# Kernel tuning notes

Measured on AMD Instinct MI355X. Metric: run time of the kernel, lower is better.

## Reference

```python
import jax, jax.numpy as jnp
import numpy as np

LN_EPS = 1e-5

def layer_norm(x, g, b):
    mu = jnp.mean(x, axis=-1, keepdims=True)
    var = jnp.var(x, axis=-1, keepdims=True)
    return (x - mu) * jax.lax.rsqrt(var + LN_EPS) * g + b

def setup_inputs() -> dict:
    key = jax.random.key(0)
    ks = jax.random.split(key, 4)
    d = 2048
    bs, win_len, obj_num = 8, 64, 36
    return {
        "visual_feats": jax.random.normal(ks[0], (bs, win_len, d), dtype=jnp.float32),
        "obj_feats": jax.random.normal(ks[1], (bs, win_len, obj_num, d), dtype=jnp.float32),
        "W_v": jax.random.normal(ks[2], (d, d), dtype=jnp.float32) * (1.0 / np.sqrt(d)),
        "b_v": jnp.zeros((d,), dtype=jnp.float32),
        "W_o": jax.random.normal(ks[3], (d, d), dtype=jnp.float32) * (1.0 / np.sqrt(d)),
        "b_o": jnp.zeros((d,), dtype=jnp.float32),
        "ln_v_g": jnp.ones((d,), dtype=jnp.float32),
        "ln_v_b": jnp.zeros((d,), dtype=jnp.float32),
        "ln_o_g": jnp.ones((d,), dtype=jnp.float32),
        "ln_o_b": jnp.zeros((d,), dtype=jnp.float32),
        "ln_ov_g": jnp.ones((d,), dtype=jnp.float32),
        "ln_ov_b": jnp.zeros((d,), dtype=jnp.float32),
    }

def reference(visual_feats, obj_feats, W_v, b_v, W_o, b_o,
              ln_v_g, ln_v_b, ln_o_g, ln_o_b, ln_ov_g, ln_ov_b):
    bs, win_len, obj_num, obj_size = obj_feats.shape
    # visual branch: linear -> tanh -> LN   [bs, F, d]
    ve = layer_norm(jnp.tanh(visual_feats @ W_v + b_v), ln_v_g, ln_v_b)
    # object branch: linear -> flatten frames*objects -> tanh -> LN  [bs, N, d]
    oe = (obj_feats @ W_o + b_o).reshape(bs, win_len * obj_num, obj_size)
    oe = layer_norm(jnp.tanh(oe), ln_o_g, ln_o_b)
    # adjacency: [bs, N, F], softmax over N (object axis, dim=1)
    adj = jnp.einsum('bnd,bfd->bnf', oe, ve) / jnp.sqrt(jnp.asarray(obj_size, dtype=oe.dtype))
    adj = jax.nn.softmax(adj, axis=1)
    # aggregate objects per frame: (oe^T @ adj)^T -> [bs, F, d]
    obj_agg = jnp.einsum('bnd,bnf->bfd', oe, adj)
    return layer_norm(jnp.tanh(obj_agg + ve), ln_ov_g, ln_ov_b)
```

## Files before the change

### kernel.cpp

```cpp
#include <hip/hip_runtime.h>
#include <cstdint>
#include <cstddef>


typedef __attribute__((ext_vector_type(4))) float f32x4;
typedef __attribute__((ext_vector_type(4))) unsigned int u32x4;
typedef __attribute__((ext_vector_type(8))) short bf16x8;

#define DD 2048
#define BS 8
#define FF 64
#define NOBJ 2304
#define MO 18432
#define MV 512

__device__ __forceinline__ unsigned short f2bf(float f) {
  unsigned int u = __float_as_uint(f);
  u += 0x7fffu + ((u >> 16) & 1u);
  return (unsigned short)(u >> 16);
}
__device__ __forceinline__ unsigned int pk2(float a, float b) {
  return (unsigned int)f2bf(a) | ((unsigned int)f2bf(b) << 16);
}

typedef __attribute__((address_space(1))) const unsigned int gas_u32;
typedef __attribute__((address_space(3))) unsigned int las_u32;
__device__ __forceinline__ void gl_lds16(const void* g, void* l) {
  __builtin_amdgcn_global_load_lds((gas_u32*)g, (las_u32*)l, 16, 0, 0);
}

__global__ __launch_bounds__(256) void k_cvt_bf16(const float* __restrict__ X,
                                                  unsigned short* __restrict__ O,
                                                  int n16) {
  int idx = blockIdx.x * 256 + threadIdx.x;
  const int stride = gridDim.x * 256;
  for (int i = idx; i < n16; i += stride) {
    const f32x4* src = (const f32x4*)(X + (size_t)i * 16);
    f32x4 a = src[0], b = src[1], c = src[2], d = src[3];
    u32x4 p = {pk2(a.x, a.y), pk2(a.z, a.w), pk2(b.x, b.y), pk2(b.z, b.w)};
    u32x4 q = {pk2(c.x, c.y), pk2(c.z, c.w), pk2(d.x, d.y), pk2(d.z, d.w)};
    u32x4* dst = (u32x4*)(O + (size_t)i * 16);
    dst[0] = p;
    dst[1] = q;
  }
}

__global__ __launch_bounds__(256) void k_wprep(const float* __restrict__ W,
                                               unsigned short* __restrict__ Wt) {
  __shared__ unsigned short sh[64][65];
  const int t = threadIdx.x;
  const int kb = blockIdx.x * 64, nb = blockIdx.y * 64;
  {
    const int rk = t >> 2, seg = t & 3;
    const float* src = W + (size_t)(kb + rk) * DD + nb + seg * 16;
#pragma unroll
    for (int q = 0; q < 4; ++q) {
      f32x4 x = *(const f32x4*)(src + q * 4);
      sh[rk][seg * 16 + q * 4 + 0] = f2bf(x.x);
      sh[rk][seg * 16 + q * 4 + 1] = f2bf(x.y);
      sh[rk][seg * 16 + q * 4 + 2] = f2bf(x.z);
      sh[rk][seg * 16 + q * 4 + 3] = f2bf(x.w);
    }
  }
  __syncthreads();
  {
    const int nn = t >> 2, ks = t & 3;
    unsigned int o[8];
#pragma unroll
    for (int j = 0; j < 8; ++j)
      o[j] = (unsigned int)sh[ks * 16 + 2 * j][nn] |
             ((unsigned int)sh[ks * 16 + 2 * j + 1][nn] << 16);
    u32x4 p0 = {o[0], o[1], o[2], o[3]};
    u32x4 p1 = {o[4], o[5], o[6], o[7]};
    unsigned short* dst = Wt + (size_t)(nb + nn) * DD + kb + ks * 16;
    ((u32x4*)dst)[0] = p0;
    ((u32x4*)dst)[1] = p1;
  }
}

__global__ __launch_bounds__(256) void k_gemm_bb(const unsigned short* __restrict__ A,
                                                 const unsigned short* __restrict__ Bt,
                                                 const float* __restrict__ bias,
                                                 float* __restrict__ Y) {
  __shared__ __align__(16) unsigned short As[128 * 32];
  __shared__ __align__(16) unsigned short Bs[128 * 32];
  const int t = threadIdx.x;
  const int lane = t & 63, wave = t >> 6;
  const int r = lane & 15, g = lane >> 4;
  const int wm = wave >> 1, wn = wave & 1;
  const int nwg = gridDim.x * gridDim.y;
  const int orig = blockIdx.y * gridDim.x + blockIdx.x;
  const int per = nwg >> 3;
  const int lin = (orig & 7) * per + (orig >> 3);
  const int bm = (lin >> 4) * 128;
  const int bn = (lin & 15) * 128;

  const int srow = t >> 2, scol = (t & 3) * 8;
  const unsigned short* agp = A + (size_t)(bm + srow) * DD + scol;
  const unsigned short* bgp = Bt + (size_t)(bn + srow) * DD + scol;
  unsigned short* alds0 = As + t * 8;
  unsigned short* alds1 = As + 2048 + t * 8;
  unsigned short* blds0 = Bs + t * 8;
  unsigned short* blds1 = Bs + 2048 + t * 8;

  f32x4 acc[4][4] = {};
  for (int kt = 0; kt < DD / 32; ++kt) {
    const int kb = kt * 32;
    gl_lds16(agp + kb, alds0);
    gl_lds16(agp + kb + (size_t)64 * DD, alds1);
    gl_lds16(bgp + kb, blds0);
    gl_lds16(bgp + kb + (size_t)64 * DD, blds1);
    __syncthreads();
    bf16x8 af[4], bfr[4];
#pragma unroll
    for (int m = 0; m < 4; ++m)
      af[m] = *(const bf16x8*)(As + (wm * 64 + m * 16 + r) * 32 + g * 8);
#pragma unroll
    for (int n = 0; n < 4; ++n)
      bfr[n] = *(const bf16x8*)(Bs + (wn * 64 + n * 16 + r) * 32 + g * 8);
#pragma unroll
    for (int m = 0; m < 4; ++m)
#pragma unroll
      for (int n = 0; n < 4; ++n)
        acc[m][n] = __builtin_amdgcn_mfma_f32_16x16x32_bf16(af[m], bfr[n], acc[m][n], 0, 0, 0);
    __syncthreads();
  }
#pragma unroll
  for (int m = 0; m < 4; ++m) {
    const int row0 = bm + wm * 64 + m * 16 + g * 4;
#pragma unroll
    for (int n = 0; n < 4; ++n) {
      const int col = bn + wn * 64 + n * 16 + r;
      const float bv = bias[col];
#pragma unroll
      for (int i = 0; i < 4; ++i)
        Y[(size_t)(row0 + i) * DD + col] = acc[m][n][i] + bv;
    }
  }
}

__global__ __launch_bounds__(256) void k_gemm_xw(const float* __restrict__ X,
                                                 const unsigned short* __restrict__ Wt,
                                                 const float* __restrict__ bias,
                                                 float* __restrict__ Y) {
  __shared__ __align__(16) unsigned short As[128 * 32];
  __shared__ __align__(16) unsigned short Bs[128 * 32];
  const int t = threadIdx.x;
  const int lane = t & 63, wave = t >> 6;
  const int r = lane & 15, g = lane >> 4;
  const int wm = wave >> 1, wn = wave & 1;
  const int bm = blockIdx.y * 128, bn = blockIdx.x * 128;
  const int arow = t >> 1, ah = t & 1;
  f32x4 acc[4][4] = {};
  const float* aptr = X + (size_t)(bm + arow) * DD + ah * 16;
  const unsigned short* bptr = Wt + (size_t)(bn + arow) * DD + ah * 16;
  for (int kt = 0; kt < DD / 32; ++kt) {
    const int kb = kt * 32;
    f32x4 a0 = *(const f32x4*)(aptr + kb);
    f32x4 a1 = *(const f32x4*)(aptr + kb + 4);
    f32x4 a2 = *(const f32x4*)(aptr + kb + 8);
    f32x4 a3 = *(const f32x4*)(aptr + kb + 12);
    u32x4 b0 = *(const u32x4*)(bptr + kb);
    u32x4 b1 = *(const u32x4*)(bptr + kb + 8);
    __syncthreads();
    u32x4 p0 = {pk2(a0.x, a0.y), pk2(a0.z, a0.w), pk2(a1.x, a1.y), pk2(a1.z, a1.w)};
    u32x4 p1 = {pk2(a2.x, a2.y), pk2(a2.z, a2.w), pk2(a3.x, a3.y), pk2(a3.z, a3.w)};
    ((u32x4*)As)[arow * 4 + ah * 2 + 0] = p0;
    ((u32x4*)As)[arow * 4 + ah * 2 + 1] = p1;
    ((u32x4*)Bs)[arow * 4 + ah * 2 + 0] = b0;
    ((u32x4*)Bs)[arow * 4 + ah * 2 + 1] = b1;
    __syncthreads();
    bf16x8 af[4], bfr[4];
#pragma unroll
    for (int m = 0; m < 4; ++m) af[m] = ((const bf16x8*)As)[(wm * 64 + m * 16 + r) * 4 + g];
#pragma unroll
    for (int n = 0; n < 4; ++n) bfr[n] = ((const bf16x8*)Bs)[(wn * 64 + n * 16 + r) * 4 + g];
#pragma unroll
    for (int m = 0; m < 4; ++m)
#pragma unroll
      for (int n = 0; n < 4; ++n)
        acc[m][n] = __builtin_amdgcn_mfma_f32_16x16x32_bf16(af[m], bfr[n], acc[m][n], 0, 0, 0);
  }
#pragma unroll
  for (int m = 0; m < 4; ++m) {
    const int row0 = bm + wm * 64 + m * 16 + g * 4;
#pragma unroll
    for (int n = 0; n < 4; ++n) {
      const int col = bn + wn * 64 + n * 16 + r;
      const float bv = bias[col];
#pragma unroll
      for (int i = 0; i < 4; ++i)
        Y[(size_t)(row0 + i) * DD + col] = acc[m][n][i] + bv;
    }
  }
}

__global__ __launch_bounds__(256) void k_ep_ln(const float* __restrict__ Y,
                                               const float* __restrict__ Y2,
                                               const float* __restrict__ gw,
                                               const float* __restrict__ bw,
                                               unsigned short* __restrict__ obf,
                                               float* __restrict__ of32) {
  const int row = blockIdx.x, t = threadIdx.x;
  const size_t base = (size_t)row * DD + t * 8;
  f32x4 v0 = ((const f32x4*)(Y + base))[0];
  f32x4 v1 = ((const f32x4*)(Y + base))[1];
  if (Y2 != nullptr) {
    v0 += ((const f32x4*)(Y2 + base))[0];
    v1 += ((const f32x4*)(Y2 + base))[1];
  }
  float tv[8];
#pragma unroll
  for (int j = 0; j < 4; ++j) {
    tv[j] = tanhf(v0[j]);
    tv[4 + j] = tanhf(v1[j]);
  }
  float s1 = 0.f, s2 = 0.f;
#pragma unroll
  for (int j = 0; j < 8; ++j) {
    s1 += tv[j];
    s2 += tv[j] * tv[j];
  }
#pragma unroll
  for (int m = 1; m < 64; m <<= 1) {
    s1 += __shfl_xor(s1, m, 64);
    s2 += __shfl_xor(s2, m, 64);
  }
  __shared__ float r1[4], r2[4];
  const int wave = t >> 6;
  if ((t & 63) == 0) {
    r1[wave] = s1;
    r2[wave] = s2;
  }
  __syncthreads();
  const float S1 = r1[0] + r1[1] + r1[2] + r1[3];
  const float S2 = r2[0] + r2[1] + r2[2] + r2[3];
  const float mean = S1 * (1.0f / DD);
  const float var = S2 * (1.0f / DD) - mean * mean;
  const float rstd = rsqrtf(var + 1e-5f);
  f32x4 g0 = ((const f32x4*)(gw + t * 8))[0], g1 = ((const f32x4*)(gw + t * 8))[1];
  f32x4 bb0 = ((const f32x4*)(bw + t * 8))[0], bb1 = ((const f32x4*)(bw + t * 8))[1];
  float o[8];
#pragma unroll
  for (int j = 0; j < 4; ++j) {
    o[j] = (tv[j] - mean) * rstd * g0[j] + bb0[j];
    o[4 + j] = (tv[4 + j] - mean) * rstd * g1[j] + bb1[j];
  }
  if (obf != nullptr) {
    u32x4 p = {pk2(o[0], o[1]), pk2(o[2], o[3]), pk2(o[4], o[5]), pk2(o[6], o[7])};
    *((u32x4*)(obf + base)) = p;
  }
  if (of32 != nullptr) {
    f32x4 w0 = {o[0], o[1], o[2], o[3]}, w1 = {o[4], o[5], o[6], o[7]};
    ((f32x4*)(of32 + base))[0] = w0;
    ((f32x4*)(of32 + base))[1] = w1;
  }
}

__global__ __launch_bounds__(256) void k_troe(const unsigned short* __restrict__ oe,
                                              unsigned short* __restrict__ oeT) {
  __shared__ unsigned short sh[64][65];
  const int t = threadIdx.x;
  const int b = blockIdx.z, nt = blockIdx.x, dt = blockIdx.y;
  {
    const int nn = t >> 2, seg = t & 3;
    const unsigned short* src = oe + ((size_t)b * NOBJ + nt * 64 + nn) * DD + dt * 64 + seg * 16;
    u32x4 x0 = ((const u32x4*)src)[0];
    u32x4 x1 = ((const u32x4*)src)[1];
    const unsigned short* px0 = (const unsigned short*)&x0;
    const unsigned short* px1 = (const unsigned short*)&x1;
#pragma unroll
    for (int j = 0; j < 8; ++j) {
      sh[nn][seg * 16 + j] = px0[j];
      sh[nn][seg * 16 + 8 + j] = px1[j];
    }
  }
  __syncthreads();
  {
    const int dd = t >> 2, ns = t & 3;
    unsigned int o[8];
#pragma unroll
    for (int j = 0; j < 8; ++j)
      o[j] = (unsigned int)sh[ns * 16 + 2 * j][dd] |
             ((unsigned int)sh[ns * 16 + 2 * j + 1][dd] << 16);
    u32x4 p0 = {o[0], o[1], o[2], o[3]};
    u32x4 p1 = {o[4], o[5], o[6], o[7]};
    unsigned short* dst = oeT + ((size_t)b * DD + dt * 64 + dd) * NOBJ + nt * 64 + ns * 16;
    ((u32x4*)dst)[0] = p0;
    ((u32x4*)dst)[1] = p1;
  }
}

__global__ __launch_bounds__(256) void k_gemm_adj(const unsigned short* __restrict__ oe,
                                                  const unsigned short* __restrict__ veb,
                                                  float* __restrict__ adjT) {
  __shared__ __align__(16) unsigned short As[128 * 32];
  __shared__ __align__(16) unsigned short Bs[64 * 32];
  const int t = threadIdx.x;
  const int lane = t & 63, wave = t >> 6;
  const int r = lane & 15, g = lane >> 4;
  const int wm = wave >> 1, wn = wave & 1;
  const int b = blockIdx.y, bm = blockIdx.x * 128;
  const int arow = t >> 1, ah = t & 1;
  const int br_ = t >> 2, bseg = t & 3;
  f32x4 acc[4][2] = {};
  const unsigned short* aptr = oe + ((size_t)b * NOBJ + bm + arow) * DD + ah * 16;
  const unsigned short* bptr = veb + ((size_t)b * FF + br_) * DD + bseg * 8;
  for (int kt = 0; kt < DD / 32; ++kt) {
    const int kb = kt * 32;
    u32x4 a0 = ((const u32x4*)(aptr + kb))[0];
    u32x4 a1 = ((const u32x4*)(aptr + kb))[1];
    u32x4 bv = *(const u32x4*)(bptr + kb);
    __syncthreads();
    ((u32x4*)As)[arow * 4 + ah * 2 + 0] = a0;
    ((u32x4*)As)[arow * 4 + ah * 2 + 1] = a1;
    ((u32x4*)Bs)[br_ * 4 + bseg] = bv;
    __syncthreads();
    bf16x8 af[4], bfr[2];
#pragma unroll
    for (int m = 0; m < 4; ++m) af[m] = ((const bf16x8*)As)[(wm * 64 + m * 16 + r) * 4 + g];
#pragma unroll
    for (int n = 0; n < 2; ++n) bfr[n] = ((const bf16x8*)Bs)[(wn * 32 + n * 16 + r) * 4 + g];
#pragma unroll
    for (int m = 0; m < 4; ++m)
#pragma unroll
      for (int n = 0; n < 2; ++n)
        acc[m][n] = __builtin_amdgcn_mfma_f32_16x16x32_bf16(af[m], bfr[n], acc[m][n], 0, 0, 0);
  }
  const float scale = 0.02209708691207961f;
#pragma unroll
  for (int m = 0; m < 4; ++m)
#pragma unroll
    for (int n = 0; n < 2; ++n) {
      const int f = wn * 32 + n * 16 + r;
      const int n0 = bm + wm * 64 + m * 16 + g * 4;
      f32x4 v = acc[m][n];
      v *= scale;
      *(f32x4*)(adjT + ((size_t)b * FF + f) * NOBJ + n0) = v;
    }
}

__global__ __launch_bounds__(256) void k_smax(const float* __restrict__ adjT,
                                              unsigned short* __restrict__ out) {
  const int t = threadIdx.x;
  const size_t base = (size_t)blockIdx.x * NOBJ;
  float v[9];
#pragma unroll
  for (int j = 0; j < 9; ++j) v[j] = adjT[base + t + j * 256];
  float m = v[0];
#pragma unroll
  for (int j = 1; j < 9; ++j) m = fmaxf(m, v[j]);
#pragma unroll
  for (int s = 1; s < 64; s <<= 1) m = fmaxf(m, __shfl_xor(m, s, 64));
  __shared__ float rm[4], rs[4];
  const int wave = t >> 6;
  if ((t & 63) == 0) rm[wave] = m;
  __syncthreads();
  m = fmaxf(fmaxf(rm[0], rm[1]), fmaxf(rm[2], rm[3]));
  float e[9];
  float s = 0.f;
#pragma unroll
  for (int j = 0; j < 9; ++j) {
    e[j] = __expf(v[j] - m);
    s += e[j];
  }
#pragma unroll
  for (int q = 1; q < 64; q <<= 1) s += __shfl_xor(s, q, 64);
  if ((t & 63) == 0) rs[wave] = s;
  __syncthreads();
  const float S = rs[0] + rs[1] + rs[2] + rs[3];
  const float inv = 1.0f / S;
#pragma unroll
  for (int j = 0; j < 9; ++j) out[base + t + j * 256] = f2bf(e[j] * inv);
}

__global__ __launch_bounds__(256) void k_gemm_agg(const unsigned short* __restrict__ adjsm,
                                                  const unsigned short* __restrict__ oeT,
                                                  float* __restrict__ agg) {
  __shared__ __align__(16) unsigned short As[64 * 32];
  __shared__ __align__(16) unsigned short Bs[128 * 32];
  const int t = threadIdx.x;
  const int lane = t & 63, wave = t >> 6;
  const int r = lane & 15, g = lane >> 4;
  const int wm = wave >> 1, wn = wave & 1;
  const int b = blockIdx.y, bn = blockIdx.x * 128;
  const int ar = t >> 2, aseg = t & 3;
  const int brow = t >> 1, bh = t & 1;
  f32x4 acc[2][4] = {};
  const unsigned short* aptr = adjsm + ((size_t)b * FF + ar) * NOBJ + aseg * 8;
  const unsigned short* bptr = oeT + ((size_t)b * DD + bn + brow) * NOBJ + bh * 16;
  for (int kt = 0; kt < NOBJ / 32; ++kt) {
    const int kb = kt * 32;
    u32x4 av = *(const u32x4*)(aptr + kb);
    u32x4 b0 = ((const u32x4*)(bptr + kb))[0];
    u32x4 b1 = ((const u32x4*)(bptr + kb))[1];
    __syncthreads();
    ((u32x4*)As)[ar * 4 + aseg] = av;
    ((u32x4*)Bs)[brow * 4 + bh * 2 + 0] = b0;
    ((u32x4*)Bs)[brow * 4 + bh * 2 + 1] = b1;
    __syncthreads();
    bf16x8 af[2], bfr[4];
#pragma unroll
    for (int m = 0; m < 2; ++m) af[m] = ((const bf16x8*)As)[(wm * 32 + m * 16 + r) * 4 + g];
#pragma unroll
    for (int n = 0; n < 4; ++n) bfr[n] = ((const bf16x8*)Bs)[(wn * 64 + n * 16 + r) * 4 + g];
#pragma unroll
    for (int m = 0; m < 2; ++m)
#pragma unroll
      for (int n = 0; n < 4; ++n)
        acc[m][n] = __builtin_amdgcn_mfma_f32_16x16x32_bf16(af[m], bfr[n], acc[m][n], 0, 0, 0);
  }
#pragma unroll
  for (int m = 0; m < 2; ++m)
#pragma unroll
    for (int n = 0; n < 4; ++n) {
      const int d = bn + wn * 64 + n * 16 + r;
#pragma unroll
      for (int i = 0; i < 4; ++i) {
        const int f = wm * 32 + m * 16 + g * 4 + i;
        agg[((size_t)b * FF + f) * DD + d] = acc[m][n][i];
      }
    }
}


extern "C" void kernel_launch(void* const* d_in, const int* in_sizes, int n_in,
                              void* d_out, int out_size, void* d_ws, size_t ws_size,
                              hipStream_t stream) {
  (void)in_sizes; (void)n_in; (void)out_size;
  const float* visual = (const float*)d_in[0];
  const float* obj    = (const float*)d_in[1];
  const float* W_v    = (const float*)d_in[2];
  const float* b_v    = (const float*)d_in[3];
  const float* W_o    = (const float*)d_in[4];
  const float* b_o    = (const float*)d_in[5];
  const float* ln_v_g = (const float*)d_in[6];
  const float* ln_v_b = (const float*)d_in[7];
  const float* ln_o_g = (const float*)d_in[8];
  const float* ln_o_b = (const float*)d_in[9];
  const float* ln_ov_g = (const float*)d_in[10];
  const float* ln_ov_b = (const float*)d_in[11];

  char* ws = (char*)d_ws;
  constexpr size_t OFF_WVT = 0;
  constexpr size_t OFF_WOT = 8ull << 20;
  constexpr size_t OFF_OBJB = 16ull << 20;
  constexpr size_t OFF_YO  = 88ull << 20;
  constexpr size_t OFF_YV  = 232ull << 20;
  constexpr size_t OFF_VEF = 236ull << 20;
  constexpr size_t OFF_VEB = 240ull << 20;
  constexpr size_t OFF_ADJ = 242ull << 20;
  constexpr size_t OFF_ADJS = OFF_ADJ + 4718592ull;
  constexpr size_t OFF_AGG = OFF_ADJS + 2359296ull;
  constexpr size_t WS_NEED = OFF_AGG + 4194304ull;
  if (ws_size < WS_NEED) return;

  unsigned short* WvT  = (unsigned short*)(ws + OFF_WVT);
  unsigned short* WoT  = (unsigned short*)(ws + OFF_WOT);
  unsigned short* objb = (unsigned short*)(ws + OFF_OBJB);
  unsigned short* oe_b = (unsigned short*)(ws + OFF_OBJB);
  float* Yo            = (float*)(ws + OFF_YO);
  unsigned short* oeT  = (unsigned short*)(ws + OFF_YO);
  float* Yv            = (float*)(ws + OFF_YV);
  float* ve_f          = (float*)(ws + OFF_VEF);
  unsigned short* ve_b = (unsigned short*)(ws + OFF_VEB);
  float* adjT          = (float*)(ws + OFF_ADJ);
  unsigned short* adjs = (unsigned short*)(ws + OFF_ADJS);
  float* agg           = (float*)(ws + OFF_AGG);

  dim3 b256(256);
  k_wprep<<<dim3(32, 32), b256, 0, stream>>>(W_v, WvT);
  k_wprep<<<dim3(32, 32), b256, 0, stream>>>(W_o, WoT);
  k_cvt_bf16<<<dim3(2048), b256, 0, stream>>>(obj, objb, MO * DD / 16);
  k_gemm_xw<<<dim3(16, MV / 128), b256, 0, stream>>>(visual, WvT, b_v, Yv);
  k_gemm_bb<<<dim3(16, MO / 128), b256, 0, stream>>>(objb, WoT, b_o, Yo);
  k_ep_ln<<<dim3(MV), b256, 0, stream>>>(Yv, nullptr, ln_v_g, ln_v_b, ve_b, ve_f);
  k_ep_ln<<<dim3(MO), b256, 0, stream>>>(Yo, nullptr, ln_o_g, ln_o_b, oe_b, nullptr);
  k_troe<<<dim3(36, 32, 8), b256, 0, stream>>>(oe_b, oeT);
  k_gemm_adj<<<dim3(NOBJ / 128, BS), b256, 0, stream>>>(oe_b, ve_b, adjT);
  k_smax<<<dim3(MV), b256, 0, stream>>>(adjT, adjs);
  k_gemm_agg<<<dim3(DD / 128, BS), b256, 0, stream>>>(adjs, oeT, agg);
  k_ep_ln<<<dim3(MV), b256, 0, stream>>>(agg, ve_f, ln_ov_g, ln_ov_b, nullptr, (float*)d_out);
}
```

Before: 461.6 us.

## Triple-buffer the object GEMM with swizzled LDS and larger 256x128 tiles

Rewrites the main bf16 object-projection GEMM to use 512-thread blocks over 256x128 output tiles with K-step 64. Global-to-LDS loads are triple-buffered and issued two stages ahead, with explicit vmcnt waits and a single barrier per iteration, so memory traffic overlaps the MFMA work. The LDS layout is XOR-swizzled to avoid bank conflicts, and wave priority is raised around the MFMA block. In exchange the kernel uses about 144KB of LDS, which limits it to one block per CU, and it depends on hand-tuned waitcnt counts being correct.

```diff
diff --git a/kernel.cpp b/kernel.cpp
--- a/kernel.cpp
+++ b/kernel.cpp
@@ -78,63 +78,103 @@
   }
 }
 
-__global__ __launch_bounds__(256) void k_gemm_bb(const unsigned short* __restrict__ A,
-                                                 const unsigned short* __restrict__ Bt,
-                                                 const float* __restrict__ bias,
-                                                 float* __restrict__ Y) {
-  __shared__ __align__(16) unsigned short As[128 * 32];
-  __shared__ __align__(16) unsigned short Bs[128 * 32];
-  const int t = threadIdx.x;
-  const int lane = t & 63, wave = t >> 6;
+__global__ __launch_bounds__(512, 1) void k_gemm_bb(const unsigned short* __restrict__ A,
+                                                    const unsigned short* __restrict__ Bt,
+                                                    const float* __restrict__ bias,
+                                                    float* __restrict__ Y) {
+  __shared__ __align__(16) unsigned short lds[3 * 24576];
+  const int tid = threadIdx.x;
+  const int lane = tid & 63, wave = tid >> 6;
   const int r = lane & 15, g = lane >> 4;
   const int wm = wave >> 1, wn = wave & 1;
+
   const int nwg = gridDim.x * gridDim.y;
   const int orig = blockIdx.y * gridDim.x + blockIdx.x;
   const int per = nwg >> 3;
   const int lin = (orig & 7) * per + (orig >> 3);
-  const int bm = (lin >> 4) * 128;
+  const int bm = (lin >> 4) * 256;
   const int bn = (lin & 15) * 128;
 
-  const int srow = t >> 2, scol = (t & 3) * 8;
-  const unsigned short* agp = A + (size_t)(bm + srow) * DD + scol;
-  const unsigned short* bgp = Bt + (size_t)(bn + srow) * DD + scol;
-  unsigned short* alds0 = As + t * 8;
-  unsigned short* alds1 = As + 2048 + t * 8;
-  unsigned short* blds0 = Bs + t * 8;
-  unsigned short* blds1 = Bs + 2048 + t * 8;
+  const int srow = tid >> 3;
+  const int k16s = (tid & 7) ^ (srow & 7);
+  const unsigned short* aSrc[4];
+#pragma unroll
+  for (int q = 0; q < 4; ++q)
+    aSrc[q] = A + (size_t)(bm + q * 64 + srow) * DD + k16s * 8;
+  const unsigned short* bSrc[2];
+#pragma unroll
+  for (int q = 0; q < 2; ++q)
+    bSrc[q] = Bt + (size_t)(bn + q * 64 + srow) * DD + k16s * 8;
+
+  const int rs = r & 7;
+  const int sa0 = ((0 + g) ^ rs) * 8;
+  const int sa1 = ((4 + g) ^ rs) * 8;
+  const int arow0 = wm * 64 + r;
+  const int brow0 = wn * 64 + r;
+
+  auto stage = [&](int buf, int kt) {
+    unsigned short* ab = lds + buf * 24576;
+    unsigned short* bb = ab + 16384;
+    const size_t ko = (size_t)kt * 64;
+#pragma unroll
+    for (int q = 0; q < 4; ++q)
+      gl_lds16(aSrc[q] + ko, ab + ((q * 512 + tid) << 3));
+#pragma unroll
+    for (int q = 0; q < 2; ++q)
+      gl_lds16(bSrc[q] + ko, bb + ((q * 512 + tid) << 3));
+  };
 
   f32x4 acc[4][4] = {};
-  for (int kt = 0; kt < DD / 32; ++kt) {
-    const int kb = kt * 32;
-    gl_lds16(agp + kb, alds0);
-    gl_lds16(agp + kb + (size_t)64 * DD, alds1);
-    gl_lds16(bgp + kb, blds0);
-    gl_lds16(bgp + kb + (size_t)64 * DD, blds1);
-    __syncthreads();
-    bf16x8 af[4], bfr[4];
-#pragma unroll
-    for (int m = 0; m < 4; ++m)
-      af[m] = *(const bf16x8*)(As + (wm * 64 + m * 16 + r) * 32 + g * 8);
-#pragma unroll
-    for (int n = 0; n < 4; ++n)
-      bfr[n] = *(const bf16x8*)(Bs + (wn * 64 + n * 16 + r) * 32 + g * 8);
-#pragma unroll
-    for (int m = 0; m < 4; ++m)
-#pragma unroll
-      for (int n = 0; n < 4; ++n)
-        acc[m][n] = __builtin_amdgcn_mfma_f32_16x16x32_bf16(af[m], bfr[n], acc[m][n], 0, 0, 0);
-    __syncthreads();
-  }
-#pragma unroll
-  for (int m = 0; m < 4; ++m) {
-    const int row0 = bm + wm * 64 + m * 16 + g * 4;
-#pragma unroll
-    for (int n = 0; n < 4; ++n) {
-      const int col = bn + wn * 64 + n * 16 + r;
+  stage(0, 0);
+  stage(1, 1);
+  asm volatile("s_waitcnt vmcnt(6)" ::: "memory");
+  __builtin_amdgcn_s_barrier();
+
+  for (int kt = 0; kt < DD / 64; ++kt) {
+    const int cur = kt % 3;
+    if (kt + 2 < DD / 64) stage((kt + 2) % 3, kt + 2);
+    const unsigned short* ab = lds + cur * 24576;
+    const unsigned short* bb = ab + 16384;
+    bf16x8 af[4][2], bfr[4][2];
+#pragma unroll
+    for (int mi = 0; mi < 4; ++mi) {
+      const int ro = (arow0 + mi * 16) * 64;
+      af[mi][0] = *(const bf16x8*)(ab + ro + sa0);
+      af[mi][1] = *(const bf16x8*)(ab + ro + sa1);
+    }
+#pragma unroll
+    for (int ni = 0; ni < 4; ++ni) {
+      const int ro = (brow0 + ni * 16) * 64;
+      bfr[ni][0] = *(const bf16x8*)(bb + ro + sa0);
+      bfr[ni][1] = *(const bf16x8*)(bb + ro + sa1);
+    }
+    __builtin_amdgcn_s_setprio(1);
+#pragma unroll
+    for (int mi = 0; mi < 4; ++mi)
+#pragma unroll
+      for (int ni = 0; ni < 4; ++ni) {
+        acc[mi][ni] = __builtin_amdgcn_mfma_f32_16x16x32_bf16(af[mi][0], bfr[ni][0], acc[mi][ni], 0, 0, 0);
+        acc[mi][ni] = __builtin_amdgcn_mfma_f32_16x16x32_bf16(af[mi][1], bfr[ni][1], acc[mi][ni], 0, 0, 0);
+      }
+    __builtin_amdgcn_s_setprio(0);
+    if (kt < DD / 64 - 2) {
+      asm volatile("s_waitcnt vmcnt(6)" ::: "memory");
+    } else {
+      asm volatile("s_waitcnt vmcnt(0)" ::: "memory");
+    }
+    __builtin_amdgcn_s_barrier();
+  }
+
+#pragma unroll
+  for (int mi = 0; mi < 4; ++mi) {
+    const int row0 = bm + wm * 64 + mi * 16 + g * 4;
+#pragma unroll
+    for (int ni = 0; ni < 4; ++ni) {
+      const int col = bn + wn * 64 + ni * 16 + r;
       const float bv = bias[col];
 #pragma unroll
       for (int i = 0; i < 4; ++i)
-        Y[(size_t)(row0 + i) * DD + col] = acc[m][n][i] + bv;
+        Y[(size_t)(row0 + i) * DD + col] = acc[mi][ni][i] + bv;
     }
   }
 }
@@ -473,7 +513,7 @@
   k_wprep<<<dim3(32, 32), b256, 0, stream>>>(W_o, WoT);
   k_cvt_bf16<<<dim3(2048), b256, 0, stream>>>(obj, objb, MO * DD / 16);
   k_gemm_xw<<<dim3(16, MV / 128), b256, 0, stream>>>(visual, WvT, b_v, Yv);
-  k_gemm_bb<<<dim3(16, MO / 128), b256, 0, stream>>>(objb, WoT, b_o, Yo);
+  k_gemm_bb<<<dim3(16, MO / 256), dim3(512), 0, stream>>>(objb, WoT, b_o, Yo);
   k_ep_ln<<<dim3(MV), b256, 0, stream>>>(Yv, nullptr, ln_v_g, ln_v_b, ve_b, ve_f);
   k_ep_ln<<<dim3(MO), b256, 0, stream>>>(Yo, nullptr, ln_o_g, ln_o_b, oe_b, nullptr);
   k_troe<<<dim3(36, 32, 8), b256, 0, stream>>>(oe_b, oeT);
```

After: 462.0 us. No clear change (+0.1%).

## Fuse tanh and LN partial stats into 256x256 pipelined object GEMM

Applied to the files above, without the earlier changes.

Replaces the 128x128 object-projection GEMM with a 256x256 tile, 512-thread kernel using a 4-slot global_load_lds pipeline with explicit vmcnt waits and setprio around MFMAs. Its epilogue applies bias and tanh, writes bf16 instead of fp32, and emits per-row partial sum and sum-of-squares. A lighter LN kernel then only reads bf16 values plus the partials to normalize. This cuts fp32 intermediate traffic and the reduction pass, but uses one-pass variance from bf16-rounded stores, which is slightly less precise, and 128KB LDS limits occupancy to one block.

```diff
diff --git a/kernel.cpp b/kernel.cpp
--- a/kernel.cpp
+++ b/kernel.cpp
@@ -21,6 +21,9 @@
 }
 __device__ __forceinline__ unsigned int pk2(float a, float b) {
   return (unsigned int)f2bf(a) | ((unsigned int)f2bf(b) << 16);
+}
+__device__ __forceinline__ float bf2f(unsigned short u) {
+  return __uint_as_float((unsigned int)u << 16);
 }
 
 typedef __attribute__((address_space(1))) const unsigned int gas_u32;
@@ -78,65 +81,164 @@
   }
 }
 
-__global__ __launch_bounds__(256) void k_gemm_bb(const unsigned short* __restrict__ A,
-                                                 const unsigned short* __restrict__ Bt,
-                                                 const float* __restrict__ bias,
-                                                 float* __restrict__ Y) {
-  __shared__ __align__(16) unsigned short As[128 * 32];
-  __shared__ __align__(16) unsigned short Bs[128 * 32];
-  const int t = threadIdx.x;
-  const int lane = t & 63, wave = t >> 6;
+__global__ __launch_bounds__(512, 1) void k_gemm_bbf(const unsigned short* __restrict__ A,
+                                                     const unsigned short* __restrict__ Bt,
+                                                     const float* __restrict__ bias,
+                                                     unsigned short* __restrict__ T,
+                                                     float* __restrict__ part) {
+  __shared__ __align__(16) unsigned short lds[65536];
+  const int tid = threadIdx.x;
+  const int lane = tid & 63, wave = tid >> 6;
   const int r = lane & 15, g = lane >> 4;
-  const int wm = wave >> 1, wn = wave & 1;
-  const int nwg = gridDim.x * gridDim.y;
-  const int orig = blockIdx.y * gridDim.x + blockIdx.x;
-  const int per = nwg >> 3;
-  const int lin = (orig & 7) * per + (orig >> 3);
-  const int bm = (lin >> 4) * 128;
-  const int bn = (lin & 15) * 128;
-
-  const int srow = t >> 2, scol = (t & 3) * 8;
-  const unsigned short* agp = A + (size_t)(bm + srow) * DD + scol;
-  const unsigned short* bgp = Bt + (size_t)(bn + srow) * DD + scol;
-  unsigned short* alds0 = As + t * 8;
-  unsigned short* alds1 = As + 2048 + t * 8;
-  unsigned short* blds0 = Bs + t * 8;
-  unsigned short* blds1 = Bs + 2048 + t * 8;
-
-  f32x4 acc[4][4] = {};
-  for (int kt = 0; kt < DD / 32; ++kt) {
-    const int kb = kt * 32;
-    gl_lds16(agp + kb, alds0);
-    gl_lds16(agp + kb + (size_t)64 * DD, alds1);
-    gl_lds16(bgp + kb, blds0);
-    gl_lds16(bgp + kb + (size_t)64 * DD, blds1);
-    __syncthreads();
-    bf16x8 af[4], bfr[4];
-#pragma unroll
-    for (int m = 0; m < 4; ++m)
-      af[m] = *(const bf16x8*)(As + (wm * 64 + m * 16 + r) * 32 + g * 8);
-#pragma unroll
-    for (int n = 0; n < 4; ++n)
-      bfr[n] = *(const bf16x8*)(Bs + (wn * 64 + n * 16 + r) * 32 + g * 8);
-#pragma unroll
-    for (int m = 0; m < 4; ++m)
-#pragma unroll
-      for (int n = 0; n < 4; ++n)
-        acc[m][n] = __builtin_amdgcn_mfma_f32_16x16x32_bf16(af[m], bfr[n], acc[m][n], 0, 0, 0);
-    __syncthreads();
-  }
-#pragma unroll
-  for (int m = 0; m < 4; ++m) {
-    const int row0 = bm + wm * 64 + m * 16 + g * 4;
-#pragma unroll
-    for (int n = 0; n < 4; ++n) {
-      const int col = bn + wn * 64 + n * 16 + r;
-      const float bv = bias[col];
-#pragma unroll
-      for (int i = 0; i < 4; ++i)
-        Y[(size_t)(row0 + i) * DD + col] = acc[m][n][i] + bv;
-    }
-  }
+  const int wm = wave >> 2, wn = wave & 3;
+
+  const int orig = blockIdx.y * 8 + blockIdx.x;
+  const int lin = (orig & 7) * 72 + (orig >> 3);
+  const int bm = (lin >> 3) * 256;
+  const int bn = (lin & 7) * 256;
+
+  const int srow = tid & 255;
+  const int k16a = tid >> 8;
+  const unsigned short* aS0 = A + (size_t)(bm + srow) * DD + k16a * 8;
+  const unsigned short* bS0 = Bt + (size_t)(bn + srow) * DD + k16a * 8;
+
+  auto stage = [&](int slot, int H) {
+    unsigned short* base = lds + slot * 16384;
+    const size_t ko = (size_t)H * 32;
+    gl_lds16(aS0 + ko, base + tid * 8);
+    gl_lds16(aS0 + ko + 16, base + (tid + 512) * 8);
+    gl_lds16(bS0 + ko, base + 8192 + tid * 8);
+    gl_lds16(bS0 + ko + 16, base + 8192 + (tid + 512) * 8);
+  };
+
+  const int aoff = (g * 256 + wm * 128 + r) * 8;
+  const int boff = 8192 + (g * 256 + wn * 64 + r) * 8;
+
+  f32x4 acc[8][4] = {};
+
+  stage(0, 0);
+  stage(1, 1);
+  stage(2, 2);
+  asm volatile("s_waitcnt vmcnt(8)" ::: "memory");
+  __builtin_amdgcn_s_barrier();
+
+  auto phase = [&](int P, int slotC, int slotS) {
+    if (P + 3 < 64) stage(slotS, P + 3);
+    const unsigned short* sb = lds + slotC * 16384;
+    bf16x8 af[8], bfv[4];
+#pragma unroll
+    for (int mi = 0; mi < 8; ++mi)
+      af[mi] = *(const bf16x8*)(sb + aoff + mi * 128);
+#pragma unroll
+    for (int ni = 0; ni < 4; ++ni)
+      bfv[ni] = *(const bf16x8*)(sb + boff + ni * 128);
+    __builtin_amdgcn_s_setprio(1);
+#pragma unroll
+    for (int mi = 0; mi < 8; ++mi)
+#pragma unroll
+      for (int ni = 0; ni < 4; ++ni)
+        acc[mi][ni] = __builtin_amdgcn_mfma_f32_16x16x32_bf16(af[mi], bfv[ni], acc[mi][ni], 0, 0, 0);
+    __builtin_amdgcn_s_setprio(0);
+    if (P < 61) {
+      asm volatile("s_waitcnt vmcnt(8)" ::: "memory");
+    } else if (P == 61) {
+      asm volatile("s_waitcnt vmcnt(4)" ::: "memory");
+    } else if (P == 62) {
+      asm volatile("s_waitcnt vmcnt(0)" ::: "memory");
+    }
+    if (P < 63) __builtin_amdgcn_s_barrier();
+  };
+
+  for (int p4 = 0; p4 < 64; p4 += 4) {
+    phase(p4 + 0, 0, 3);
+    phase(p4 + 1, 1, 0);
+    phase(p4 + 2, 2, 1);
+    phase(p4 + 3, 3, 2);
+  }
+
+  float bv[4];
+#pragma unroll
+  for (int ni = 0; ni < 4; ++ni) bv[ni] = bias[bn + wn * 64 + ni * 16 + r];
+  const int slot = ((lin & 7) << 2) + wn;
+#pragma unroll
+  for (int mi = 0; mi < 8; ++mi) {
+#pragma unroll
+    for (int i2 = 0; i2 < 4; ++i2) {
+      const int row = bm + wm * 128 + mi * 16 + g * 4 + i2;
+      unsigned short* trow = T + (size_t)row * DD + bn + wn * 64 + r;
+      float s1 = 0.f, s2 = 0.f;
+#pragma unroll
+      for (int ni = 0; ni < 4; ++ni) {
+        const float tv = tanhf(acc[mi][ni][i2] + bv[ni]);
+        trow[ni * 16] = f2bf(tv);
+        s1 += tv;
+        s2 += tv * tv;
+      }
+#pragma unroll
+      for (int m = 1; m < 16; m <<= 1) {
+        s1 += __shfl_xor(s1, m, 64);
+        s2 += __shfl_xor(s2, m, 64);
+      }
+      if (r == 0) {
+        float2 p2 = make_float2(s1, s2);
+        *(float2*)(part + (size_t)row * 64 + slot * 2) = p2;
+      }
+    }
+  }
+}
+
+__global__ __launch_bounds__(256) void k_ep_ln2(const unsigned short* __restrict__ T,
+                                                const float* __restrict__ part,
+                                                const float* __restrict__ gw,
+                                                const float* __restrict__ bw,
+                                                unsigned short* __restrict__ obf) {
+  const int row = blockIdx.x, t = threadIdx.x;
+  float s1 = 0.f, s2 = 0.f;
+  if (t < 32) {
+    float2 p = ((const float2*)(part + (size_t)row * 64))[t];
+    s1 = p.x;
+    s2 = p.y;
+  }
+#pragma unroll
+  for (int m = 1; m < 64; m <<= 1) {
+    s1 += __shfl_xor(s1, m, 64);
+    s2 += __shfl_xor(s2, m, 64);
+  }
+  __shared__ float sh[2];
+  if (t == 0) {
+    sh[0] = s1;
+    sh[1] = s2;
+  }
+  __syncthreads();
+  const float mean = sh[0] * (1.0f / DD);
+  const float var = sh[1] * (1.0f / DD) - mean * mean;
+  const float rstd = rsqrtf(var + 1e-5f);
+  const size_t base = (size_t)row * DD + t * 8;
+  u32x4 tin = *(const u32x4*)(T + base);
+  f32x4 g0 = ((const f32x4*)(gw + t * 8))[0], g1 = ((const f32x4*)(gw + t * 8))[1];
+  f32x4 bb0 = ((const f32x4*)(bw + t * 8))[0], bb1 = ((const f32x4*)(bw + t * 8))[1];
+  float o[8];
+#pragma unroll
+  for (int j = 0; j < 4; ++j) {
+    const float tl = bf2f((unsigned short)(tin[j] & 0xffffu));
+    const float th = bf2f((unsigned short)(tin[j] >> 16));
+    o[2 * j] = (tl - mean) * rstd * ((const float*)&g0)[0] ;
+    (void)th;
+  }
+  float gv[8], bvv[8];
+  gv[0] = g0.x; gv[1] = g0.y; gv[2] = g0.z; gv[3] = g0.w;
+  gv[4] = g1.x; gv[5] = g1.y; gv[6] = g1.z; gv[7] = g1.w;
+  bvv[0] = bb0.x; bvv[1] = bb0.y; bvv[2] = bb0.z; bvv[3] = bb0.w;
+  bvv[4] = bb1.x; bvv[5] = bb1.y; bvv[6] = bb1.z; bvv[7] = bb1.w;
+#pragma unroll
+  for (int j = 0; j < 4; ++j) {
+    const float tl = bf2f((unsigned short)(tin[j] & 0xffffu));
+    const float th = bf2f((unsigned short)(tin[j] >> 16));
+    o[2 * j] = (tl - mean) * rstd * gv[2 * j] + bvv[2 * j];
+    o[2 * j + 1] = (th - mean) * rstd * gv[2 * j + 1] + bvv[2 * j + 1];
+  }
+  u32x4 p = {pk2(o[0], o[1]), pk2(o[2], o[3]), pk2(o[4], o[5]), pk2(o[6], o[7])};
+  *((u32x4*)(obf + base)) = p;
 }
 
 __global__ __launch_bounds__(256) void k_gemm_xw(const float* __restrict__ X,
@@ -187,10 +289,10 @@
 #pragma unroll
     for (int n = 0; n < 4; ++n) {
       const int col = bn + wn * 64 + n * 16 + r;
-      const float bv = bias[col];
+      const float bvx = bias[col];
 #pragma unroll
       for (int i = 0; i < 4; ++i)
-        Y[(size_t)(row0 + i) * DD + col] = acc[m][n][i] + bv;
+        Y[(size_t)(row0 + i) * DD + col] = acc[m][n][i] + bvx;
     }
   }
 }
@@ -310,11 +412,11 @@
     const int kb = kt * 32;
     u32x4 a0 = ((const u32x4*)(aptr + kb))[0];
     u32x4 a1 = ((const u32x4*)(aptr + kb))[1];
-    u32x4 bv = *(const u32x4*)(bptr + kb);
+    u32x4 bvx = *(const u32x4*)(bptr + kb);
     __syncthreads();
     ((u32x4*)As)[arow * 4 + ah * 2 + 0] = a0;
     ((u32x4*)As)[arow * 4 + ah * 2 + 1] = a1;
-    ((u32x4*)Bs)[br_ * 4 + bseg] = bv;
+    ((u32x4*)Bs)[br_ * 4 + bseg] = bvx;
     __syncthreads();
     bf16x8 af[4], bfr[2];
 #pragma unroll
@@ -445,7 +547,8 @@
   constexpr size_t OFF_WVT = 0;
   constexpr size_t OFF_WOT = 8ull << 20;
   constexpr size_t OFF_OBJB = 16ull << 20;
-  constexpr size_t OFF_YO  = 88ull << 20;
+  constexpr size_t OFF_T   = 88ull << 20;
+  constexpr size_t OFF_PART = 160ull << 20;
   constexpr size_t OFF_YV  = 232ull << 20;
   constexpr size_t OFF_VEF = 236ull << 20;
   constexpr size_t OFF_VEB = 240ull << 20;
@@ -459,8 +562,9 @@
   unsigned short* WoT  = (unsigned short*)(ws + OFF_WOT);
   unsigned short* objb = (unsigned short*)(ws + OFF_OBJB);
   unsigned short* oe_b = (unsigned short*)(ws + OFF_OBJB);
-  float* Yo            = (float*)(ws + OFF_YO);
-  unsigned short* oeT  = (unsigned short*)(ws + OFF_YO);
+  unsigned short* T    = (unsigned short*)(ws + OFF_T);
+  unsigned short* oeT  = (unsigned short*)(ws + OFF_T);
+  float* part          = (float*)(ws + OFF_PART);
   float* Yv            = (float*)(ws + OFF_YV);
   float* ve_f          = (float*)(ws + OFF_VEF);
   unsigned short* ve_b = (unsigned short*)(ws + OFF_VEB);
@@ -473,9 +577,9 @@
   k_wprep<<<dim3(32, 32), b256, 0, stream>>>(W_o, WoT);
   k_cvt_bf16<<<dim3(2048), b256, 0, stream>>>(obj, objb, MO * DD / 16);
   k_gemm_xw<<<dim3(16, MV / 128), b256, 0, stream>>>(visual, WvT, b_v, Yv);
-  k_gemm_bb<<<dim3(16, MO / 128), b256, 0, stream>>>(objb, WoT, b_o, Yo);
+  k_gemm_bbf<<<dim3(8, MO / 256), dim3(512), 0, stream>>>(objb, WoT, b_o, T, part);
   k_ep_ln<<<dim3(MV), b256, 0, stream>>>(Yv, nullptr, ln_v_g, ln_v_b, ve_b, ve_f);
-  k_ep_ln<<<dim3(MO), b256, 0, stream>>>(Yo, nullptr, ln_o_g, ln_o_b, oe_b, nullptr);
+  k_ep_ln2<<<dim3(MO), b256, 0, stream>>>(T, part, ln_o_g, ln_o_b, oe_b);
   k_troe<<<dim3(36, 32, 8), b256, 0, stream>>>(oe_b, oeT);
   k_gemm_adj<<<dim3(NOBJ / 128, BS), b256, 0, stream>>>(oe_b, ve_b, adjT);
   k_smax<<<dim3(MV), b256, 0, stream>>>(adjT, adjs);
```

After: 589.9 us. +27.8%, slower.
